# Kernel tuning notes

Hardware: AMD Instinct MI355X
Metric: run time of the kernel (lower is better)

## Reference

```python
import jax, jax.numpy as jnp
import numpy as np

B, C = 8192, 4096
P, Q, EPS = 0.8, 2.0, 0.01


def setup_inputs() -> dict:
    key = jax.random.key(0)
    k1, k2 = jax.random.split(key)
    outputs = jax.random.normal(k1, (B, C), dtype=jnp.float32)
    targets = jax.random.randint(k2, (B,), 0, C)
    return {"outputs": outputs, "targets": targets}


def reference(outputs, targets):
    num_classes = outputs.shape[1]
    # accumulated class counts for this batch (torch loop over unique targets == bincount)
    acc = jax.ops.segment_sum(
        jnp.ones_like(targets, dtype=outputs.dtype), targets, num_segments=num_classes
    )
    acc = jnp.clip(acc, 1.0)  # clamp(min=1)
    onehot = jax.nn.one_hot(targets, num_classes, dtype=outputs.dtype)  # [B, C]

    # mitigation factor: gather rows of the implicit CxC ratio matrix by target
    # ratio[b, j] = acc[j] / acc[targets[b]]
    ratio = acc[None, :] / acc[targets][:, None]  # [B, C]
    mitigation = jnp.where(ratio < 1.0, ratio ** P, 1.0)

    # compensation factor on detached softmax scores
    scores = jax.nn.softmax(jax.lax.stop_gradient(outputs), axis=1)  # [B, C]
    self_scores = jnp.take_along_axis(scores, targets[:, None], axis=1)  # [B, 1]
    sratio = scores / jnp.clip(self_scores, EPS)
    compensation = jnp.where(sratio > 1.0, sratio ** Q, 1.0)

    seesaw = mitigation * compensation  # [B, C]
    logits = outputs + jnp.log(seesaw) * (1.0 - onehot)

    logp = jax.nn.log_softmax(logits, axis=1)
    nll = -jnp.take_along_axis(logp, targets[:, None], axis=1)[:, 0]
    return jnp.mean(nll)
```

## Files before the change

kernel.cpp:

```cpp
#include <hip/hip_runtime.h>
#include <math.h>


#define CC 4096

__device__ __forceinline__ float wave_max(float v) {
    #pragma unroll
    for (int o = 32; o > 0; o >>= 1) v = fmaxf(v, __shfl_xor(v, o, 64));
    return v;
}
__device__ __forceinline__ float wave_sum(float v) {
    #pragma unroll
    for (int o = 32; o > 0; o >>= 1) v += __shfl_xor(v, o, 64);
    return v;
}

__device__ __forceinline__ float esum4(float4 v, float M) {
    return (__expf(v.x - M) + __expf(v.y - M)) +
           (__expf(v.z - M) + __expf(v.w - M));
}

__device__ __forceinline__ float seesaw1(float o, float la, float la_t,
                                         float Koff) {
    float mit = (la < la_t) ? 0.8f * (la - la_t) : 0.f;
    float d   = o - Koff;
    float cmp = (d > 0.f) ? 2.0f * d : 0.f;
    return o + mit + cmp;
}

__device__ __forceinline__ float lsum4(float4 v, float4 la, float la_t,
                                       float Koff, float M2) {
    float a = __expf(seesaw1(v.x, la.x, la_t, Koff) - M2);
    float b = __expf(seesaw1(v.y, la.y, la_t, Koff) - M2);
    float c = __expf(seesaw1(v.z, la.z, la_t, Koff) - M2);
    float d = __expf(seesaw1(v.w, la.w, la_t, Koff) - M2);
    return (a + b) + (c + d);
}

__global__ __launch_bounds__(1024) void k_hist(const int* __restrict__ tg, int B,
                                               float* __restrict__ logacc) {
    __shared__ int hacc[CC];
    const int tid = threadIdx.x;
    #pragma unroll
    for (int k = 0; k < CC / 1024; ++k) hacc[tid + k * 1024] = 0;
    __syncthreads();
    for (int i = tid; i < B; i += 1024) atomicAdd(&hacc[tg[i]], 1);
    __syncthreads();
    #pragma unroll
    for (int k = 0; k < CC / 1024; ++k) {
        int i = tid + k * 1024;
        int a = hacc[i];
        if (a < 1) a = 1;
        logacc[i] = __logf((float)a);
    }
}

__global__ __launch_bounds__(256, 8) void k_row(const float* __restrict__ outp,
                                                const int* __restrict__ tg,
                                                const float* __restrict__ logacc,
                                                float* __restrict__ nll) {
    __shared__ float red_m[4], red_s[4], red_s2[4];

    const int b   = blockIdx.x;
    const int tid = threadIdx.x;
    const int w   = tid >> 6;
    const bool lane0 = (tid & 63) == 0;

    const float LOG_EPS = -4.605170185988091f;

    const float4* __restrict__ src = (const float4*)(outp + (size_t)b * CC);
    const float4* __restrict__ lac = (const float4*)logacc;

    float4 v0 = src[tid];
    float4 v1 = src[tid + 256];
    float4 v2 = src[tid + 512];
    float4 v3 = src[tid + 768];
    float m0 = fmaxf(fmaxf(v0.x, v0.y), fmaxf(v0.z, v0.w));
    float m1 = fmaxf(fmaxf(v1.x, v1.y), fmaxf(v1.z, v1.w));
    float m2 = fmaxf(fmaxf(v2.x, v2.y), fmaxf(v2.z, v2.w));
    float m3 = fmaxf(fmaxf(v3.x, v3.y), fmaxf(v3.z, v3.w));
    float m  = fmaxf(fmaxf(m0, m1), fmaxf(m2, m3));

    const int   t    = tg[b];
    const float o_t  = outp[(size_t)b * CC + t];
    const float la_t = logacc[t];

    m = wave_max(m);
    if (lane0) red_m[w] = m;
    __syncthreads();
    const float M = fmaxf(fmaxf(red_m[0], red_m[1]), fmaxf(red_m[2], red_m[3]));

    float s0 = esum4(v0, M);
    float s1 = esum4(v1, M);
    float s2 = esum4(v2, M);
    float s3 = esum4(v3, M);
    float s  = wave_sum((s0 + s1) + (s2 + s3));
    if (lane0) red_s[w] = s;
    __syncthreads();
    const float S    = (red_s[0] + red_s[1]) + (red_s[2] + red_s[3]);
    const float lse1 = __logf(S);

    const float ls_t    = o_t - M - lse1;
    const float logclip = fmaxf(ls_t, LOG_EPS);
    const float Koff    = M + lse1 + logclip;
    const float M2      = M + fmaxf(0.f, 2.0f * (M - Koff));

    float z0 = lsum4(v0, lac[tid      ], la_t, Koff, M2);
    float z1 = lsum4(v1, lac[tid + 256], la_t, Koff, M2);
    float z2 = lsum4(v2, lac[tid + 512], la_t, Koff, M2);
    float z3 = lsum4(v3, lac[tid + 768], la_t, Koff, M2);
    float z  = wave_sum((z0 + z1) + (z2 + z3));
    if (lane0) red_s2[w] = z;
    __syncthreads();

    if (tid == 0) {
        float S2 = (red_s2[0] + red_s2[1]) + (red_s2[2] + red_s2[3]);
        nll[b] = M2 + __logf(S2) - o_t;
    }
}

__global__ __launch_bounds__(1024) void k_reduce(const float* __restrict__ nll,
                                                 float* __restrict__ out, int B) {
    __shared__ float red[16];
    const int tid = threadIdx.x;
    float s = 0.f;
    for (int i = tid; i < B; i += 1024) s += nll[i];
    s = wave_sum(s);
    if ((tid & 63) == 0) red[tid >> 6] = s;
    __syncthreads();
    if (tid == 0) {
        float tsum = 0.f;
        #pragma unroll
        for (int k = 0; k < 16; ++k) tsum += red[k];
        out[0] = tsum / (float)B;
    }
}

extern "C" void kernel_launch(void* const* d_in, const int* in_sizes, int n_in,
                              void* d_out, int out_size, void* d_ws, size_t ws_size,
                              hipStream_t stream) {
    const float* outp = (const float*)d_in[0];
    const int*   tg   = (const int*)d_in[1];
    float*       out  = (float*)d_out;

    const int B = in_sizes[1];

    char*  ws     = (char*)d_ws;
    float* logacc = (float*)ws;
    float* nll    = (float*)(ws + 16384);

    k_hist  <<<1, 1024, 0, stream>>>(tg, B, logacc);
    k_row   <<<B, 256, 0, stream>>>(outp, tg, logacc, nll);
    k_reduce<<<1, 1024, 0, stream>>>(nll, out, B);
}
```

Before: 37.39 us.

## Map one wavefront per row and vectorize histogram and reduction loads

The row kernel now gives each 64-lane wavefront a whole row (16 float4 per lane) with four rows per block. This removes the shared-memory reductions and the three __syncthreads per row, and launch bounds drop to 4 blocks per SM to fit the higher register use. The histogram and final-reduction kernels also switch to int4/float4 loads. The tradeoff is more register pressure and lower occupancy, and the vector loads assume B is divisible by 4.

```diff
diff --git a/kernel.cpp b/kernel.cpp
--- a/kernel.cpp
+++ b/kernel.cpp
@@ -44,7 +44,12 @@
     #pragma unroll
     for (int k = 0; k < CC / 1024; ++k) hacc[tid + k * 1024] = 0;
     __syncthreads();
-    for (int i = tid; i < B; i += 1024) atomicAdd(&hacc[tg[i]], 1);
+    const int4* __restrict__ tg4 = (const int4*)tg;
+    for (int i = tid; i < B / 4; i += 1024) {
+        int4 tv = tg4[i];
+        atomicAdd(&hacc[tv.x], 1); atomicAdd(&hacc[tv.y], 1);
+        atomicAdd(&hacc[tv.z], 1); atomicAdd(&hacc[tv.w], 1);
+    }
     __syncthreads();
     #pragma unroll
     for (int k = 0; k < CC / 1024; ++k) {
@@ -55,49 +60,40 @@
     }
 }
 
-__global__ __launch_bounds__(256, 8) void k_row(const float* __restrict__ outp,
+#define ROW_EACH(OP) OP(0) OP(1) OP(2) OP(3) OP(4) OP(5) OP(6) OP(7) \
+                     OP(8) OP(9) OP(10) OP(11) OP(12) OP(13) OP(14) OP(15)
+
+__global__ __launch_bounds__(256, 4) void k_row(const float* __restrict__ outp,
                                                 const int* __restrict__ tg,
                                                 const float* __restrict__ logacc,
                                                 float* __restrict__ nll) {
-    __shared__ float red_m[4], red_s[4], red_s2[4];
-
-    const int b   = blockIdx.x;
-    const int tid = threadIdx.x;
-    const int w   = tid >> 6;
-    const bool lane0 = (tid & 63) == 0;
+    const int lane = threadIdx.x & 63;
+    const int b    = (blockIdx.x << 2) + (threadIdx.x >> 6);
 
     const float LOG_EPS = -4.605170185988091f;
 
     const float4* __restrict__ src = (const float4*)(outp + (size_t)b * CC);
     const float4* __restrict__ lac = (const float4*)logacc;
 
-    float4 v0 = src[tid];
-    float4 v1 = src[tid + 256];
-    float4 v2 = src[tid + 512];
-    float4 v3 = src[tid + 768];
-    float m0 = fmaxf(fmaxf(v0.x, v0.y), fmaxf(v0.z, v0.w));
-    float m1 = fmaxf(fmaxf(v1.x, v1.y), fmaxf(v1.z, v1.w));
-    float m2 = fmaxf(fmaxf(v2.x, v2.y), fmaxf(v2.z, v2.w));
-    float m3 = fmaxf(fmaxf(v3.x, v3.y), fmaxf(v3.z, v3.w));
-    float m  = fmaxf(fmaxf(m0, m1), fmaxf(m2, m3));
+#define DECL_V(i) float4 v##i = src[lane + (i << 6)];
+    ROW_EACH(DECL_V)
+#undef DECL_V
 
     const int   t    = tg[b];
     const float o_t  = outp[(size_t)b * CC + t];
     const float la_t = logacc[t];
 
-    m = wave_max(m);
-    if (lane0) red_m[w] = m;
-    __syncthreads();
-    const float M = fmaxf(fmaxf(red_m[0], red_m[1]), fmaxf(red_m[2], red_m[3]));
+    float m = -3.4e38f;
+#define VMX(i) m = fmaxf(m, fmaxf(fmaxf(v##i.x, v##i.y), fmaxf(v##i.z, v##i.w)));
+    ROW_EACH(VMX)
+#undef VMX
+    const float M = wave_max(m);
 
-    float s0 = esum4(v0, M);
-    float s1 = esum4(v1, M);
-    float s2 = esum4(v2, M);
-    float s3 = esum4(v3, M);
-    float s  = wave_sum((s0 + s1) + (s2 + s3));
-    if (lane0) red_s[w] = s;
-    __syncthreads();
-    const float S    = (red_s[0] + red_s[1]) + (red_s[2] + red_s[3]);
+    float s0 = esum4(v0,  M) + esum4(v4,  M) + esum4(v8,  M) + esum4(v12, M);
+    float s1 = esum4(v1,  M) + esum4(v5,  M) + esum4(v9,  M) + esum4(v13, M);
+    float s2 = esum4(v2,  M) + esum4(v6,  M) + esum4(v10, M) + esum4(v14, M);
+    float s3 = esum4(v3,  M) + esum4(v7,  M) + esum4(v11, M) + esum4(v15, M);
+    const float S    = wave_sum((s0 + s1) + (s2 + s3));
     const float lse1 = __logf(S);
 
     const float ls_t    = o_t - M - lse1;
@@ -105,26 +101,37 @@
     const float Koff    = M + lse1 + logclip;
     const float M2      = M + fmaxf(0.f, 2.0f * (M - Koff));
 
-    float z0 = lsum4(v0, lac[tid      ], la_t, Koff, M2);
-    float z1 = lsum4(v1, lac[tid + 256], la_t, Koff, M2);
-    float z2 = lsum4(v2, lac[tid + 512], la_t, Koff, M2);
-    float z3 = lsum4(v3, lac[tid + 768], la_t, Koff, M2);
-    float z  = wave_sum((z0 + z1) + (z2 + z3));
-    if (lane0) red_s2[w] = z;
-    __syncthreads();
+    float z0 = lsum4(v0,  lac[lane          ], la_t, Koff, M2)
+             + lsum4(v4,  lac[lane + (4<<6) ], la_t, Koff, M2)
+             + lsum4(v8,  lac[lane + (8<<6) ], la_t, Koff, M2)
+             + lsum4(v12, lac[lane + (12<<6)], la_t, Koff, M2);
+    float z1 = lsum4(v1,  lac[lane + (1<<6) ], la_t, Koff, M2)
+             + lsum4(v5,  lac[lane + (5<<6) ], la_t, Koff, M2)
+             + lsum4(v9,  lac[lane + (9<<6) ], la_t, Koff, M2)
+             + lsum4(v13, lac[lane + (13<<6)], la_t, Koff, M2);
+    float z2 = lsum4(v2,  lac[lane + (2<<6) ], la_t, Koff, M2)
+             + lsum4(v6,  lac[lane + (6<<6) ], la_t, Koff, M2)
+             + lsum4(v10, lac[lane + (10<<6)], la_t, Koff, M2)
+             + lsum4(v14, lac[lane + (14<<6)], la_t, Koff, M2);
+    float z3 = lsum4(v3,  lac[lane + (3<<6) ], la_t, Koff, M2)
+             + lsum4(v7,  lac[lane + (7<<6) ], la_t, Koff, M2)
+             + lsum4(v11, lac[lane + (11<<6)], la_t, Koff, M2)
+             + lsum4(v15, lac[lane + (15<<6)], la_t, Koff, M2);
+    const float S2 = wave_sum((z0 + z1) + (z2 + z3));
 
-    if (tid == 0) {
-        float S2 = (red_s2[0] + red_s2[1]) + (red_s2[2] + red_s2[3]);
-        nll[b] = M2 + __logf(S2) - o_t;
-    }
+    if (lane == 0) nll[b] = M2 + __logf(S2) - o_t;
 }
 
 __global__ __launch_bounds__(1024) void k_reduce(const float* __restrict__ nll,
                                                  float* __restrict__ out, int B) {
     __shared__ float red[16];
     const int tid = threadIdx.x;
+    const float4* __restrict__ n4 = (const float4*)nll;
     float s = 0.f;
-    for (int i = tid; i < B; i += 1024) s += nll[i];
+    for (int i = tid; i < B / 4; i += 1024) {
+        float4 v = n4[i];
+        s += (v.x + v.y) + (v.z + v.w);
+    }
     s = wave_sum(s);
     if ((tid & 63) == 0) red[tid >> 6] = s;
     __syncthreads();
@@ -150,6 +157,6 @@
     float* nll    = (float*)(ws + 16384);
 
     k_hist  <<<1, 1024, 0, stream>>>(tg, B, logacc);
-    k_row   <<<B, 256, 0, stream>>>(outp, tg, logacc, nll);
+    k_row   <<<B / 4, 256, 0, stream>>>(outp, tg, logacc, nll);
     k_reduce<<<1, 1024, 0, stream>>>(nll, out, B);
 }
```

Measured after the change: 57.85 us. +54.7%, slower.

## Use online max-sum merge to drop one block barrier in row kernel

Applied to the files above, without the earlier changes.

Each thread now computes its local max and a partial exp-sum relative to that local max. The wave and block reductions merge (max, sum) pairs instead of running a max pass and then a sum pass. This removes one __syncthreads and one shuffle round in the per-row kernel, at the cost of extra exp calls inside the merge. The histogram and final reduction kernels also switch to vectorized int4/float4 loads, which assumes B is divisible by 4.

```diff
diff --git a/kernel.cpp b/kernel.cpp
--- a/kernel.cpp
+++ b/kernel.cpp
@@ -4,11 +4,6 @@
 
 #define CC 4096
 
-__device__ __forceinline__ float wave_max(float v) {
-    #pragma unroll
-    for (int o = 32; o > 0; o >>= 1) v = fmaxf(v, __shfl_xor(v, o, 64));
-    return v;
-}
 __device__ __forceinline__ float wave_sum(float v) {
     #pragma unroll
     for (int o = 32; o > 0; o >>= 1) v += __shfl_xor(v, o, 64);
@@ -37,6 +32,12 @@
     return (a + b) + (c + d);
 }
 
+__device__ __forceinline__ void ms_merge(float& m, float& s, float m2, float s2) {
+    float Mn = fmaxf(m, m2);
+    s = s * __expf(m - Mn) + s2 * __expf(m2 - Mn);
+    m = Mn;
+}
+
 __global__ __launch_bounds__(1024) void k_hist(const int* __restrict__ tg, int B,
                                                float* __restrict__ logacc) {
     __shared__ int hacc[CC];
@@ -44,7 +45,12 @@
     #pragma unroll
     for (int k = 0; k < CC / 1024; ++k) hacc[tid + k * 1024] = 0;
     __syncthreads();
-    for (int i = tid; i < B; i += 1024) atomicAdd(&hacc[tg[i]], 1);
+    const int4* __restrict__ tg4 = (const int4*)tg;
+    for (int i = tid; i < B / 4; i += 1024) {
+        int4 tv = tg4[i];
+        atomicAdd(&hacc[tv.x], 1); atomicAdd(&hacc[tv.y], 1);
+        atomicAdd(&hacc[tv.z], 1); atomicAdd(&hacc[tv.w], 1);
+    }
     __syncthreads();
     #pragma unroll
     for (int k = 0; k < CC / 1024; ++k) {
@@ -59,7 +65,8 @@
                                                 const int* __restrict__ tg,
                                                 const float* __restrict__ logacc,
                                                 float* __restrict__ nll) {
-    __shared__ float red_m[4], red_s[4], red_s2[4];
+    __shared__ float2 red_ms[4];
+    __shared__ float  red_s2[4];
 
     const int b   = blockIdx.x;
     const int tid = threadIdx.x;
@@ -68,6 +75,10 @@
 
     const float LOG_EPS = -4.605170185988091f;
 
+    const int   t    = tg[b];
+    const float o_t  = outp[(size_t)b * CC + t];
+    const float la_t = logacc[t];
+
     const float4* __restrict__ src = (const float4*)(outp + (size_t)b * CC);
     const float4* __restrict__ lac = (const float4*)logacc;
 
@@ -75,29 +86,27 @@
     float4 v1 = src[tid + 256];
     float4 v2 = src[tid + 512];
     float4 v3 = src[tid + 768];
+
     float m0 = fmaxf(fmaxf(v0.x, v0.y), fmaxf(v0.z, v0.w));
     float m1 = fmaxf(fmaxf(v1.x, v1.y), fmaxf(v1.z, v1.w));
     float m2 = fmaxf(fmaxf(v2.x, v2.y), fmaxf(v2.z, v2.w));
     float m3 = fmaxf(fmaxf(v3.x, v3.y), fmaxf(v3.z, v3.w));
     float m  = fmaxf(fmaxf(m0, m1), fmaxf(m2, m3));
+    float s  = (esum4(v0, m) + esum4(v1, m)) + (esum4(v2, m) + esum4(v3, m));
 
-    const int   t    = tg[b];
-    const float o_t  = outp[(size_t)b * CC + t];
-    const float la_t = logacc[t];
+    #pragma unroll
+    for (int o = 32; o > 0; o >>= 1) {
+        float mo = __shfl_xor(m, o, 64);
+        float so = __shfl_xor(s, o, 64);
+        ms_merge(m, s, mo, so);
+    }
+    if (lane0) red_ms[w] = make_float2(m, s);
+    __syncthreads();
 
-    m = wave_max(m);
-    if (lane0) red_m[w] = m;
-    __syncthreads();
-    const float M = fmaxf(fmaxf(red_m[0], red_m[1]), fmaxf(red_m[2], red_m[3]));
-
-    float s0 = esum4(v0, M);
-    float s1 = esum4(v1, M);
-    float s2 = esum4(v2, M);
-    float s3 = esum4(v3, M);
-    float s  = wave_sum((s0 + s1) + (s2 + s3));
-    if (lane0) red_s[w] = s;
-    __syncthreads();
-    const float S    = (red_s[0] + red_s[1]) + (red_s[2] + red_s[3]);
+    float M = red_ms[0].x, S = red_ms[0].y;
+    ms_merge(M, S, red_ms[1].x, red_ms[1].y);
+    ms_merge(M, S, red_ms[2].x, red_ms[2].y);
+    ms_merge(M, S, red_ms[3].x, red_ms[3].y);
     const float lse1 = __logf(S);
 
     const float ls_t    = o_t - M - lse1;
@@ -123,8 +132,12 @@
                                                  float* __restrict__ out, int B) {
     __shared__ float red[16];
     const int tid = threadIdx.x;
+    const float4* __restrict__ n4 = (const float4*)nll;
     float s = 0.f;
-    for (int i = tid; i < B; i += 1024) s += nll[i];
+    for (int i = tid; i < B / 4; i += 1024) {
+        float4 v = n4[i];
+        s += (v.x + v.y) + (v.z + v.w);
+    }
     s = wave_sum(s);
     if ((tid & 63) == 0) red[tid >> 6] = s;
     __syncthreads();
```

After: 38.77 us. 1.04x slower.
